# Kernel optimization log

Hardware: AMD Instinct MI355X
Metric: run time of the kernel (lower is better)

## Reference

```python
import jax, jax.numpy as jnp
import numpy as np

B, S, D, H, HD = 1, 2048, 3072, 24, 128
FFN = int(D / 3 * 8)  # 8192
ADALN = 256
NORM_EPS = 1e-6
QK_EPS = 1e-5
AXES_DIMS = (16, 56, 56)
AXES_LENS = (64, 128, 128)
THETA = 256.0


def rmsnorm(x, w, eps):
    var = jnp.mean(jnp.square(x), axis=-1, keepdims=True)
    return x * jax.lax.rsqrt(var + eps) * w


def apply_rope(x, cos, sin):
    # x: [B,S,H,HD]; cos/sin: [B,S,HD//2] (broadcast over heads, matching freqs_cis.unsqueeze(2))
    xr = x[..., 0::2]
    xi = x[..., 1::2]
    c = cos[:, :, None, :]
    s = sin[:, :, None, :]
    or_ = xr * c - xi * s
    oi_ = xr * s + xi * c
    return jnp.stack([or_, oi_], axis=-1).reshape(x.shape)


def rope_angles(ids):
    # ids: [B,S,3] int; returns angles [B,S,HD//2] concatenated per axis like RopeEmbedder
    parts = []
    for d, idx_axis in zip(AXES_DIMS, range(len(AXES_DIMS))):
        freqs = 1.0 / (THETA ** (jnp.arange(0, d, 2, dtype=jnp.float32) / d))  # [d/2]
        ang = ids[..., idx_axis].astype(jnp.float32)[..., None] * freqs  # [B,S,d/2]
        parts.append(ang)
    return jnp.concatenate(parts, axis=-1)  # [B,S,64]


def setup_inputs() -> dict:
    key = jax.random.key(0)
    ks = jax.random.split(key, 20)
    w = 0.02
    ids = jnp.concatenate([
        jax.random.randint(ks[15], (B, S, 1), 0, AXES_LENS[0]),
        jax.random.randint(ks[16], (B, S, 1), 0, AXES_LENS[1]),
        jax.random.randint(ks[17], (B, S, 1), 0, AXES_LENS[2]),
    ], axis=-1)
    return {
        "x": jax.random.normal(ks[0], (B, S, D), jnp.float32),
        "adaln_input": jax.random.normal(ks[1], (B, ADALN), jnp.float32),
        "attn_mask": jnp.ones((B, S), dtype=bool),
        "ids": ids,
        "attn_norm1_w": jnp.ones((D,), jnp.float32),
        "attn_norm2_w": jnp.ones((D,), jnp.float32),
        "ffn_norm1_w": jnp.ones((D,), jnp.float32),
        "ffn_norm2_w": jnp.ones((D,), jnp.float32),
        "norm_q_w": jnp.ones((HD,), jnp.float32),
        "norm_k_w": jnp.ones((HD,), jnp.float32),
        "wq": jax.random.normal(ks[2], (D, D), jnp.float32) * w,
        "wk": jax.random.normal(ks[3], (D, D), jnp.float32) * w,
        "wv": jax.random.normal(ks[4], (D, D), jnp.float32) * w,
        "wo": jax.random.normal(ks[5], (D, D), jnp.float32) * w,
        "w1": jax.random.normal(ks[6], (D, FFN), jnp.float32) * w,
        "w2": jax.random.normal(ks[7], (FFN, D), jnp.float32) * w,
        "w3": jax.random.normal(ks[8], (D, FFN), jnp.float32) * w,
        "adaln_w": jax.random.normal(ks[9], (ADALN, 4 * D), jnp.float32) * w,
        "adaln_b": jnp.zeros((4 * D,), jnp.float32),
    }


def block_forward(x, adaln_input, attn_mask, ids,
                  attn_norm1_w, attn_norm2_w, ffn_norm1_w, ffn_norm2_w,
                  norm_q_w, norm_k_w, wq, wk, wv, wo, w1, w2, w3,
                  adaln_w, adaln_b):
    ang = rope_angles(ids)
    cos, sin = jnp.cos(ang), jnp.sin(ang)

    mod = adaln_input @ adaln_w + adaln_b
    scale_msa, gate_msa, scale_mlp, gate_mlp = jnp.split(mod[:, None, :], 4, axis=2)
    gate_msa, gate_mlp = jnp.tanh(gate_msa), jnp.tanh(gate_mlp)
    scale_msa, scale_mlp = 1.0 + scale_msa, 1.0 + scale_mlp

    # Attention branch
    xs = rmsnorm(x, attn_norm1_w, NORM_EPS) * scale_msa  # [B,S,D]
    q = (xs @ wq).reshape(B, S, H, HD)
    k = (xs @ wk).reshape(B, S, H, HD)
    v = (xs @ wv).reshape(B, S, H, HD)
    q = rmsnorm(q, norm_q_w, QK_EPS)
    k = rmsnorm(k, norm_k_w, QK_EPS)
    q = apply_rope(q, cos, sin)
    k = apply_rope(k, cos, sin)

    scores = jnp.einsum('bqhd,bkhd->bhqk', q, k) / jnp.sqrt(jnp.float32(HD))
    neg = jnp.finfo(scores.dtype).min
    scores = jnp.where(attn_mask[:, None, None, :], scores, neg)
    probs = jax.nn.softmax(scores, axis=-1)
    attn = jnp.einsum('bhqk,bkhd->bqhd', probs, v).reshape(B, S, D)
    attn_out = attn @ wo

    x = x + gate_msa * rmsnorm(attn_out, attn_norm2_w, NORM_EPS)

    # FFN branch (SwiGLU)
    xf = rmsnorm(x, ffn_norm1_w, NORM_EPS) * scale_mlp
    h = jax.nn.silu(xf @ w1) * (xf @ w3)
    ffn_out = h @ w2
    x = x + gate_mlp * rmsnorm(ffn_out, ffn_norm2_w, NORM_EPS)
    return x


def reference(x, adaln_input, attn_mask, ids,
              attn_norm1_w, attn_norm2_w, ffn_norm1_w, ffn_norm2_w,
              norm_q_w, norm_k_w, wq, wk, wv, wo, w1, w2, w3,
              adaln_w, adaln_b):
    return block_forward(x, adaln_input, attn_mask, ids,
                         attn_norm1_w, attn_norm2_w, ffn_norm1_w, ffn_norm2_w,
                         norm_q_w, norm_k_w, wq, wk, wv, wo, w1, w2, w3,
                         adaln_w, adaln_b)
```

## Files before the change

### kernel.cpp

```cpp
#include <hip/hip_runtime.h>

#define AS1 __attribute__((address_space(1)))
#define AS3 __attribute__((address_space(3)))

typedef __bf16 bf16;
using bf16x8 = __attribute__((ext_vector_type(8))) __bf16;
using bf16x4 = __attribute__((ext_vector_type(4))) __bf16;
using bf16x2 = __attribute__((ext_vector_type(2))) __bf16;
using f32x4  = __attribute__((ext_vector_type(4))) float;


__device__ inline float wsum(float v) {
#pragma unroll
  for (int o = 32; o; o >>= 1) v += __shfl_xor(v, o, 64);
  return v;
}

template <int EPI>
__global__ __launch_bounds__(512, 1) void gemm256(
    const bf16* __restrict__ A, const bf16* __restrict__ Bt, void* __restrict__ Cv,
    int K, int lda, int ldb, int ldc, long long kOff, long long sC) {
  __shared__ bf16 lds[2][2][256 * 64];
  const int t = threadIdx.x;
  const int lane = t & 63, wid = t >> 6;
  const int wm = wid >> 2, wn = wid & 3;
  const int row16 = lane & 15, kg = lane >> 4;
  const int m0 = blockIdx.x * 256, n0 = blockIdx.y * 256;
  const int NT = K >> 6;
  const int sgran = (lane & 7) ^ (lane >> 3);
  A += (long long)blockIdx.z * kOff;
  Bt += (long long)blockIdx.z * kOff;

  auto stageA = [&](int buf, int r, int tk) {
    const int wrow = ((wid & 4) << 5) + (r << 5) + ((wid & 3) << 3);
    __builtin_amdgcn_global_load_lds(
        (const AS1 void*)(A + (long long)(m0 + wrow + (lane >> 3)) * lda + tk * 64 +
                          (sgran << 3)),
        (AS3 void*)&lds[buf][0][wrow * 64], 16, 0, 0);
  };
  auto stageB = [&](int buf, int r, int tk) {
    const int wrow = ((wid & 4) << 5) + (r << 5) + ((wid & 3) << 3);
    __builtin_amdgcn_global_load_lds(
        (const AS1 void*)(Bt + (long long)(n0 + wrow + (lane >> 3)) * ldb + tk * 64 +
                          (sgran << 3)),
        (AS3 void*)&lds[buf][1][wrow * 64], 16, 0, 0);
  };

  f32x4 acc[8][4];
#pragma unroll
  for (int i = 0; i < 8; ++i)
#pragma unroll
    for (int j = 0; j < 4; ++j) acc[i][j] = (f32x4){0.f, 0.f, 0.f, 0.f};

#pragma unroll
  for (int r = 0; r < 4; ++r) { stageA(0, r, 0); stageB(0, r, 0); }
#pragma unroll
  for (int r = 0; r < 3; ++r) { stageA(1, r, 1); stageB(1, r, 1); }

  bf16x8 bfr[4][2], af[2][2];

  for (int kt = 0; kt < NT; ++kt) {
    const int cb = kt & 1, nb = cb ^ 1;
    if (kt + 1 < NT) asm volatile("s_waitcnt vmcnt(6)" ::: "memory");
    else             asm volatile("s_waitcnt vmcnt(0)" ::: "memory");
    __builtin_amdgcn_s_barrier();

    if (kt + 1 < NT) { stageA(nb, 3, kt + 1); stageB(nb, 3, kt + 1); }
#pragma unroll
    for (int ni = 0; ni < 4; ++ni)
#pragma unroll
      for (int kk = 0; kk < 2; ++kk) {
        const int r = wn * 64 + ni * 16 + row16;
        bfr[ni][kk] = *(const bf16x8*)&lds[cb][1][r * 64 + (((kk * 4 + kg) ^ (r & 7)) << 3)];
      }
#pragma unroll
    for (int mi = 0; mi < 2; ++mi)
#pragma unroll
      for (int kk = 0; kk < 2; ++kk) {
        const int r = wm * 128 + mi * 16 + row16;
        af[mi][kk] = *(const bf16x8*)&lds[cb][0][r * 64 + (((kk * 4 + kg) ^ (r & 7)) << 3)];
      }
    asm volatile("s_waitcnt lgkmcnt(0)" ::: "memory");
    __builtin_amdgcn_s_setprio(1);
#pragma unroll
    for (int kk = 0; kk < 2; ++kk)
#pragma unroll
      for (int mi = 0; mi < 2; ++mi)
#pragma unroll
        for (int ni = 0; ni < 4; ++ni)
          acc[mi][ni] =
              __builtin_amdgcn_mfma_f32_16x16x32_bf16(af[mi][kk], bfr[ni][kk], acc[mi][ni], 0, 0, 0);
    __builtin_amdgcn_s_setprio(0);

#pragma unroll
    for (int q = 1; q < 4; ++q) {
      __builtin_amdgcn_s_barrier();
      if (kt + 2 < NT) { stageA(cb, q - 1, kt + 2); stageB(cb, q - 1, kt + 2); }
#pragma unroll
      for (int mi = 0; mi < 2; ++mi)
#pragma unroll
        for (int kk = 0; kk < 2; ++kk) {
          const int r = wm * 128 + q * 32 + mi * 16 + row16;
          af[mi][kk] = *(const bf16x8*)&lds[cb][0][r * 64 + (((kk * 4 + kg) ^ (r & 7)) << 3)];
        }
      asm volatile("s_waitcnt lgkmcnt(0)" ::: "memory");
      __builtin_amdgcn_s_setprio(1);
#pragma unroll
      for (int kk = 0; kk < 2; ++kk)
#pragma unroll
        for (int mi = 0; mi < 2; ++mi)
#pragma unroll
          for (int ni = 0; ni < 4; ++ni)
            acc[q * 2 + mi][ni] = __builtin_amdgcn_mfma_f32_16x16x32_bf16(
                af[mi][kk], bfr[ni][kk], acc[q * 2 + mi][ni], 0, 0, 0);
      __builtin_amdgcn_s_setprio(0);
    }
  }

  float* Cf = (float*)Cv;
  bf16* Cb = (bf16*)Cv;
  const long long cz = (long long)blockIdx.z * sC;
#pragma unroll
  for (int mf = 0; mf < 8; ++mf)
#pragma unroll
    for (int ni = 0; ni < 4; ++ni)
#pragma unroll
      for (int rr = 0; rr < 4; ++rr) {
        const int row = m0 + wm * 128 + (mf >> 1) * 32 + (mf & 1) * 16 + kg * 4 + rr;
        const int col = n0 + wn * 64 + ni * 16 + row16;
        const float v = acc[mf][ni][rr];
        if constexpr (EPI == 2) {
          const float other = __shfl_xor(v, 1, 64);
          if ((row16 & 1) == 0) {
            const float sl = v / (1.f + __expf(-v));
            Cb[cz + (long long)row * ldc + (col >> 1)] = (bf16)(sl * other);
          }
        } else {
          const long long idx = cz + (long long)row * ldc + col;
          if constexpr (EPI == 0) Cf[idx] = v;
          else Cb[idx] = (bf16)v;
        }
      }
}

template <int EPI>
__global__ __launch_bounds__(512, 1) void gemm192(
    const bf16* __restrict__ A, const bf16* __restrict__ Bt, void* __restrict__ Cv,
    int K, int lda, int ldb, int ldc, long long kOff, long long sC) {
  __shared__ bf16 lds[2][448 * 64];
  const int t = threadIdx.x;
  const int lane = t & 63, wid = t >> 6;
  const int wm = wid >> 2, wn = wid & 3;
  const int row16 = lane & 15, kg = lane >> 4;
  const int m0 = blockIdx.x * 256, n0 = blockIdx.y * 192;
  const int NT = K >> 6;
  const int sgran = (lane & 7) ^ (lane >> 3);
  A += (long long)blockIdx.z * kOff;
  Bt += (long long)blockIdx.z * kOff;

  auto stageA = [&](int buf, int r, int tk) {
    const int wrow = ((wid & 4) << 5) + (r << 5) + ((wid & 3) << 3);
    __builtin_amdgcn_global_load_lds(
        (const AS1 void*)(A + (long long)(m0 + wrow + (lane >> 3)) * lda + tk * 64 +
                          (sgran << 3)),
        (AS3 void*)&lds[buf][wrow * 64], 16, 0, 0);
  };
  auto stageB = [&](int buf, int r, int tk) {
    const int wrow = r * 64 + wid * 8;
    __builtin_amdgcn_global_load_lds(
        (const AS1 void*)(Bt + (long long)(n0 + wrow + (lane >> 3)) * ldb + tk * 64 +
                          (sgran << 3)),
        (AS3 void*)&lds[buf][(256 + wrow) * 64], 16, 0, 0);
  };

  f32x4 acc[8][3];
#pragma unroll
  for (int i = 0; i < 8; ++i)
#pragma unroll
    for (int j = 0; j < 3; ++j) acc[i][j] = (f32x4){0.f, 0.f, 0.f, 0.f};

#pragma unroll
  for (int r = 0; r < 4; ++r) stageA(0, r, 0);
#pragma unroll
  for (int r = 0; r < 3; ++r) stageB(0, r, 0);
#pragma unroll
  for (int r = 0; r < 3; ++r) { stageA(1, r, 1); stageB(1, r, 1); }

  bf16x8 bfr[3][2], af[2][2];

  for (int kt = 0; kt < NT; ++kt) {
    const int cb = kt & 1, nb = cb ^ 1;
    if (kt + 1 < NT) asm volatile("s_waitcnt vmcnt(6)" ::: "memory");
    else             asm volatile("s_waitcnt vmcnt(0)" ::: "memory");
    __builtin_amdgcn_s_barrier();

    if (kt + 1 < NT) stageA(nb, 3, kt + 1);
#pragma unroll
    for (int ni = 0; ni < 3; ++ni)
#pragma unroll
      for (int kk = 0; kk < 2; ++kk) {
        const int r = wn * 48 + ni * 16 + row16;
        bfr[ni][kk] =
            *(const bf16x8*)&lds[cb][(256 + r) * 64 + (((kk * 4 + kg) ^ (r & 7)) << 3)];
      }
#pragma unroll
    for (int mi = 0; mi < 2; ++mi)
#pragma unroll
      for (int kk = 0; kk < 2; ++kk) {
        const int r = wm * 128 + mi * 16 + row16;
        af[mi][kk] = *(const bf16x8*)&lds[cb][r * 64 + (((kk * 4 + kg) ^ (r & 7)) << 3)];
      }
    __builtin_amdgcn_s_barrier();
    asm volatile("s_waitcnt lgkmcnt(0)" ::: "memory");
    __builtin_amdgcn_s_setprio(1);
#pragma unroll
    for (int kk = 0; kk < 2; ++kk)
#pragma unroll
      for (int mi = 0; mi < 2; ++mi)
#pragma unroll
        for (int ni = 0; ni < 3; ++ni)
          acc[mi][ni] =
              __builtin_amdgcn_mfma_f32_16x16x32_bf16(af[mi][kk], bfr[ni][kk], acc[mi][ni], 0, 0, 0);
    __builtin_amdgcn_s_setprio(0);

#pragma unroll
    for (int q = 1; q < 4; ++q) {
      __builtin_amdgcn_s_barrier();
      if (kt + 2 < NT) { stageA(cb, q - 1, kt + 2); stageB(cb, q - 1, kt + 2); }
#pragma unroll
      for (int mi = 0; mi < 2; ++mi)
#pragma unroll
        for (int kk = 0; kk < 2; ++kk) {
          const int r = wm * 128 + q * 32 + mi * 16 + row16;
          af[mi][kk] = *(const bf16x8*)&lds[cb][r * 64 + (((kk * 4 + kg) ^ (r & 7)) << 3)];
        }
      __builtin_amdgcn_s_barrier();
      asm volatile("s_waitcnt lgkmcnt(0)" ::: "memory");
      __builtin_amdgcn_s_setprio(1);
#pragma unroll
      for (int kk = 0; kk < 2; ++kk)
#pragma unroll
        for (int mi = 0; mi < 2; ++mi)
#pragma unroll
          for (int ni = 0; ni < 3; ++ni)
            acc[q * 2 + mi][ni] = __builtin_amdgcn_mfma_f32_16x16x32_bf16(
                af[mi][kk], bfr[ni][kk], acc[q * 2 + mi][ni], 0, 0, 0);
      __builtin_amdgcn_s_setprio(0);
    }
  }

  float* Cf = (float*)Cv;
  bf16* Cb = (bf16*)Cv;
  const long long cz = (long long)blockIdx.z * sC;
#pragma unroll
  for (int mf = 0; mf < 8; ++mf)
#pragma unroll
    for (int ni = 0; ni < 3; ++ni)
#pragma unroll
      for (int rr = 0; rr < 4; ++rr) {
        const int row = m0 + wm * 128 + (mf >> 1) * 32 + (mf & 1) * 16 + kg * 4 + rr;
        const int col = n0 + wn * 48 + ni * 16 + row16;
        const long long idx = cz + (long long)row * ldc + col;
        const float v = acc[mf][ni][rr];
        if constexpr (EPI == 0) Cf[idx] = v;
        else Cb[idx] = (bf16)v;
      }
}

__global__ __launch_bounds__(256) void flash_attn_k(const bf16* __restrict__ qkv,
                                                    const bf16* __restrict__ vt,
                                                    bf16* __restrict__ Opb,
                                                    float* __restrict__ mlp) {
  __shared__ bf16 Ks[64 * 128];
  __shared__ bf16 Vs[128 * 64];
  __shared__ bf16 Ps[4 * 32 * 64];
  const int t = threadIdx.x, lane = t & 63, wid = t >> 6;
  const int row16 = lane & 15, kg = lane >> 4;
  const int q0 = blockIdx.x * 128;
  const int h = blockIdx.y;
  const int z = blockIdx.z;
  const bf16* Qp = qkv + h * 128;
  const bf16* Kp = qkv + 3072 + h * 128;
  const bf16* Vt = vt + (long long)h * 262144;
  const float iscale = 0.08838834764831845f;

  bf16x8 qf[2][4];
#pragma unroll
  for (int mi = 0; mi < 2; ++mi)
#pragma unroll
    for (int kc = 0; kc < 4; ++kc)
      qf[mi][kc] = *(const bf16x8*)&Qp[(long long)(q0 + wid * 32 + mi * 16 + row16) * 9216 +
                                       kc * 32 + kg * 8];
  bf16x8 ones;
#pragma unroll
  for (int j = 0; j < 8; ++j) ones[j] = (bf16)1.0f;

  f32x4 oacc[2][8];
#pragma unroll
  for (int mi = 0; mi < 2; ++mi)
#pragma unroll
    for (int nd = 0; nd < 8; ++nd) oacc[mi][nd] = (f32x4){0.f, 0.f, 0.f, 0.f};
  f32x4 lacc[2] = {(f32x4){0.f, 0.f, 0.f, 0.f}, (f32x4){0.f, 0.f, 0.f, 0.f}};
  float mst[2][4];
#pragma unroll
  for (int mi = 0; mi < 2; ++mi)
#pragma unroll
    for (int r = 0; r < 4; ++r) mst[mi][r] = -1e30f;

  bf16* Pw = &Ps[wid * 2048];
  const int kvbase = z << 10;

  for (int kv0 = kvbase; kv0 < kvbase + 1024; kv0 += 64) {
#pragma unroll
    for (int p = 0; p < 4; ++p) {
      const int gi = p * 256 + t;
      const int row = gi >> 4, g = gi & 15;
      __builtin_amdgcn_global_load_lds(
          (const AS1 void*)(Kp + (long long)(kv0 + row) * 9216 + ((g ^ (row & 7)) << 3)),
          (AS3 void*)&Ks[(p * 256 + wid * 64) * 8], 16, 0, 0);
    }
#pragma unroll
    for (int p = 0; p < 4; ++p) {
      const int gi = p * 256 + t;
      const int row = gi >> 3, g = gi & 7;
      __builtin_amdgcn_global_load_lds(
          (const AS1 void*)(Vt + (long long)row * 2048 + kv0 + ((g ^ (row & 7)) << 3)),
          (AS3 void*)&Vs[(p * 256 + wid * 64) * 8], 16, 0, 0);
    }
    __syncthreads();

    f32x4 sacc[2][4];
#pragma unroll
    for (int mi = 0; mi < 2; ++mi)
#pragma unroll
      for (int nf = 0; nf < 4; ++nf) sacc[mi][nf] = (f32x4){0.f, 0.f, 0.f, 0.f};
#pragma unroll
    for (int kc = 0; kc < 4; ++kc) {
      bf16x8 kf[4];
#pragma unroll
      for (int nf = 0; nf < 4; ++nf) {
        const int row = nf * 16 + row16;
        kf[nf] = *(const bf16x8*)&Ks[(row * 16 + ((kc * 4 + kg) ^ (row & 7))) * 8];
      }
#pragma unroll
      for (int mi = 0; mi < 2; ++mi)
#pragma unroll
        for (int nf = 0; nf < 4; ++nf)
          sacc[mi][nf] =
              __builtin_amdgcn_mfma_f32_16x16x32_bf16(qf[mi][kc], kf[nf], sacc[mi][nf], 0, 0, 0);
    }

    float fac[2][4];
#pragma unroll
    for (int mi = 0; mi < 2; ++mi)
#pragma unroll
      for (int r = 0; r < 4; ++r) {
        float rm = sacc[mi][0][r];
#pragma unroll
        for (int nf = 1; nf < 4; ++nf) rm = fmaxf(rm, sacc[mi][nf][r]);
        rm = fmaxf(rm, __shfl_xor(rm, 1, 64));
        rm = fmaxf(rm, __shfl_xor(rm, 2, 64));
        rm = fmaxf(rm, __shfl_xor(rm, 4, 64));
        rm = fmaxf(rm, __shfl_xor(rm, 8, 64));
        const float mnew = fmaxf(mst[mi][r], rm * iscale);
        fac[mi][r] = __expf(mst[mi][r] - mnew);
        mst[mi][r] = mnew;
#pragma unroll
        for (int nf = 0; nf < 4; ++nf)
          sacc[mi][nf][r] = __expf(sacc[mi][nf][r] * iscale - mnew);
      }
#pragma unroll
    for (int mi = 0; mi < 2; ++mi)
#pragma unroll
      for (int r = 0; r < 4; ++r) {
        lacc[mi][r] *= fac[mi][r];
#pragma unroll
        for (int nd = 0; nd < 8; ++nd) oacc[mi][nd][r] *= fac[mi][r];
      }

#pragma unroll
    for (int mi = 0; mi < 2; ++mi)
#pragma unroll
      for (int nf = 0; nf < 4; ++nf)
#pragma unroll
        for (int r = 0; r < 4; ++r) {
          const int row = mi * 16 + kg * 4 + r;
          const int col = nf * 16 + row16;
          Pw[(row * 8 + ((col >> 3) ^ (row & 7))) * 8 + (col & 7)] = (bf16)sacc[mi][nf][r];
        }

#pragma unroll
    for (int kvc = 0; kvc < 2; ++kvc) {
      bf16x8 pf[2], vf[8];
#pragma unroll
      for (int mi = 0; mi < 2; ++mi) {
        const int row = mi * 16 + row16;
        pf[mi] = *(const bf16x8*)&Pw[(row * 8 + ((kvc * 4 + kg) ^ (row & 7))) * 8];
      }
#pragma unroll
      for (int nd = 0; nd < 8; ++nd) {
        const int row = nd * 16 + row16;
        vf[nd] = *(const bf16x8*)&Vs[(row * 8 + ((kvc * 4 + kg) ^ (row & 7))) * 8];
      }
#pragma unroll
      for (int mi = 0; mi < 2; ++mi) {
        lacc[mi] = __builtin_amdgcn_mfma_f32_16x16x32_bf16(pf[mi], ones, lacc[mi], 0, 0, 0);
#pragma unroll
        for (int nd = 0; nd < 8; ++nd)
          oacc[mi][nd] =
              __builtin_amdgcn_mfma_f32_16x16x32_bf16(pf[mi], vf[nd], oacc[mi][nd], 0, 0, 0);
      }
    }
    __syncthreads();
  }

  bf16* Oz = Opb + (long long)z * 6291456;
#pragma unroll
  for (int mi = 0; mi < 2; ++mi)
#pragma unroll
    for (int nd = 0; nd < 8; ++nd)
#pragma unroll
      for (int r = 0; r < 4; ++r) {
        const int row = q0 + wid * 32 + mi * 16 + kg * 4 + r;
        const int col = h * 128 + nd * 16 + row16;
        Oz[(long long)row * 3072 + col] = (bf16)oacc[mi][nd][r];
      }
  if (row16 == 0) {
#pragma unroll
    for (int mi = 0; mi < 2; ++mi)
#pragma unroll
      for (int r = 0; r < 4; ++r) {
        const int s = q0 + wid * 32 + mi * 16 + kg * 4 + r;
        const long long mi2 = ((long long)z * 49152 + s * 24 + h) * 2;
        mlp[mi2] = mst[mi][r];
        mlp[mi2 + 1] = lacc[mi][r];
      }
  }
}

__global__ __launch_bounds__(256) void fa_combine_k(const bf16* __restrict__ Opb,
                                                    const float* __restrict__ mlp,
                                                    bf16* __restrict__ attn) {
  const int t = threadIdx.x, lane = t & 63, wid = t >> 6;
  const int pair = blockIdx.x * 4 + wid;
  const int s = pair / 24, h = pair % 24;
  const float2 ml0 = *(const float2*)&mlp[(long long)pair * 2];
  const float2 ml1 = *(const float2*)&mlp[(49152LL + pair) * 2];
  const float m = fmaxf(ml0.x, ml1.x);
  const float a0 = __expf(ml0.x - m), a1 = __expf(ml1.x - m);
  const float inv = 1.f / (ml0.y * a0 + ml1.y * a1);
  const long long base = (long long)s * 3072 + h * 128 + lane * 2;
  const bf16x2 o0 = *(const bf16x2*)&Opb[base];
  const bf16x2 o1 = *(const bf16x2*)&Opb[6291456LL + base];
  bf16x2 o;
  o[0] = (bf16)(((float)o0[0] * a0 + (float)o1[0] * a1) * inv);
  o[1] = (bf16)(((float)o0[1] * a0 + (float)o1[1] * a1) * inv);
  *(bf16x2*)&attn[base] = o;
}

__device__ inline void convT_tile(const float* __restrict__ in, bf16* __restrict__ out,
                                  int R, int C, int bx, int by, int rmul, int roff) {
  __shared__ float tile[64][65];
  const int t = threadIdx.x;
  const int r0 = by * 64, c0 = bx * 64;
#pragma unroll
  for (int it = 0; it < 4; ++it) {
    const int idx = it * 256 + t;
    const int rl = idx >> 4, c4 = (idx & 15) << 2;
    const float4 v = *(const float4*)&in[(long long)(r0 + rl) * C + c0 + c4];
    tile[rl][c4 + 0] = v.x;
    tile[rl][c4 + 1] = v.y;
    tile[rl][c4 + 2] = v.z;
    tile[rl][c4 + 3] = v.w;
  }
  __syncthreads();
#pragma unroll
  for (int it = 0; it < 4; ++it) {
    const int idx = it * 256 + t;
    const int cl = idx >> 4, r4 = (idx & 15) << 2;
    bf16x4 o;
    o[0] = (bf16)tile[r4 + 0][cl];
    o[1] = (bf16)tile[r4 + 1][cl];
    o[2] = (bf16)tile[r4 + 2][cl];
    o[3] = (bf16)tile[r4 + 3][cl];
    *(bf16x4*)&out[(long long)((c0 + cl) * rmul + roff) * R + r0 + r4] = o;
  }
}

__global__ __launch_bounds__(256) void convAll(
    const float* __restrict__ wq, const float* __restrict__ wk,
    const float* __restrict__ wv, const float* __restrict__ wo,
    const float* __restrict__ w1, const float* __restrict__ w3,
    const float* __restrict__ w2, bf16* __restrict__ wqkvT, bf16* __restrict__ woT,
    bf16* __restrict__ w13T, bf16* __restrict__ w2T) {
  const int id = blockIdx.x;
  if (id < 9216) {
    const int m = id / 2304, l = id % 2304;
    const float* in = m == 0 ? wq : m == 1 ? wk : m == 2 ? wv : wo;
    bf16* out = m < 3 ? wqkvT + (long long)m * 9437184 : woT;
    convT_tile(in, out, 3072, 3072, l % 48, l / 48, 1, 0);
  } else if (id < 21504) {
    int l = id - 9216;
    const int m = l / 6144;
    l %= 6144;
    convT_tile(m ? w3 : w1, w13T, 3072, 8192, l % 128, l / 128, 2, m);
  } else {
    const int l = id - 21504;
    convT_tile(w2, w2T, 8192, 3072, l % 48, l / 48, 1, 0);
  }
}

__global__ __launch_bounds__(256) void ropetab_k(const int* __restrict__ ids,
                                                 float* __restrict__ cosT,
                                                 float* __restrict__ sinT) {
  const int i = blockIdx.x * 256 + threadIdx.x;
  const int s = i >> 6, j = i & 63;
  int ax, fi;
  float d;
  if (j < 8) { ax = 0; fi = j; d = 16.f; }
  else if (j < 36) { ax = 1; fi = j - 8; d = 56.f; }
  else { ax = 2; fi = j - 36; d = 56.f; }
  const float freq = exp2f(-16.f * (float)fi / d);
  const float ang = (float)ids[s * 3 + ax] * freq;
  cosT[i] = cosf(ang);
  sinT[i] = sinf(ang);
}

__global__ __launch_bounds__(256) void adaln_kernel(const float* __restrict__ ain,
                                                    const float* __restrict__ W,
                                                    const float* __restrict__ b,
                                                    float* __restrict__ out) {
  __shared__ float a[256];
  const int t = threadIdx.x;
  a[t] = ain[t];
  __syncthreads();
  const int n = blockIdx.x * 256 + t;
  float acc = b[n];
  for (int k = 0; k < 256; ++k) acc = fmaf(a[k], W[(long long)k * 12288 + n], acc);
  const int chunk = n / 3072;
  out[n] = (chunk & 1) ? tanhf(acc) : (1.f + acc);
}

__global__ __launch_bounds__(256) void rmsnorm_scale_k(const float* __restrict__ x,
                                                       const float* __restrict__ w,
                                                       const float* __restrict__ scale,
                                                       bf16* __restrict__ out) {
  __shared__ float red[4];
  const int t = threadIdx.x, lane = t & 63, wid = t >> 6;
  const long long base = (long long)blockIdx.x * 3072;
  float v[12];
  float ss = 0.f;
#pragma unroll
  for (int ch = 0; ch < 3; ++ch) {
    const float4 f = *(const float4*)&x[base + ch * 1024 + t * 4];
    v[ch * 4 + 0] = f.x; v[ch * 4 + 1] = f.y; v[ch * 4 + 2] = f.z; v[ch * 4 + 3] = f.w;
    ss += f.x * f.x + f.y * f.y + f.z * f.z + f.w * f.w;
  }
  ss = wsum(ss);
  if (!lane) red[wid] = ss;
  __syncthreads();
  const float r = rsqrtf((red[0] + red[1] + red[2] + red[3]) / 3072.f + 1e-6f);
#pragma unroll
  for (int ch = 0; ch < 3; ++ch) {
    const int col = ch * 1024 + t * 4;
    bf16x4 o;
#pragma unroll
    for (int j = 0; j < 4; ++j) o[j] = (bf16)(v[ch * 4 + j] * r * w[col + j] * scale[col + j]);
    *(bf16x4*)&out[base + col] = o;
  }
}

__global__ __launch_bounds__(256) void qknorm_rope_k(bf16* __restrict__ qkv,
                                                     const float* __restrict__ cosT,
                                                     const float* __restrict__ sinT,
                                                     const float* __restrict__ wq,
                                                     const float* __restrict__ wk) {
  const int t = threadIdx.x, lane = t & 63, wid = t >> 6;
  const int idx = blockIdx.x * 4 + wid;
  const int s = idx / 24, h = idx % 24;
  const int isK = blockIdx.y;
  bf16* base = qkv + (long long)s * 9216 + isK * 3072 + h * 128;
  bf16x2 p = *(const bf16x2*)(base + 2 * lane);
  float xr = (float)p[0], xi = (float)p[1];
  const float ss = wsum(xr * xr + xi * xi);
  const float r = rsqrtf(ss / 128.f + 1e-5f);
  const float* w = isK ? wk : wq;
  const float2 wv = *(const float2*)&w[2 * lane];
  xr *= r * wv.x;
  xi *= r * wv.y;
  const float c = cosT[s * 64 + lane], sn = sinT[s * 64 + lane];
  bf16x2 o;
  o[0] = (bf16)(xr * c - xi * sn);
  o[1] = (bf16)(xr * sn + xi * c);
  *(bf16x2*)(base + 2 * lane) = o;
}

__global__ __launch_bounds__(256) void vtrans_k(const bf16* __restrict__ qkv,
                                                bf16* __restrict__ vt) {
  __shared__ bf16 tile[64][72];
  const int t = threadIdx.x;
  const int s0 = blockIdx.x * 64, d0 = blockIdx.y * 64, h = blockIdx.z;
#pragma unroll
  for (int it = 0; it < 2; ++it) {
    const int idx = it * 256 + t;
    const int sl = idx >> 3, c8 = (idx & 7) << 3;
    const bf16x8 v =
        *(const bf16x8*)&qkv[(long long)(s0 + sl) * 9216 + 6144 + h * 128 + d0 + c8];
    *(bf16x8*)&tile[sl][c8] = v;
  }
  __syncthreads();
#pragma unroll
  for (int it = 0; it < 2; ++it) {
    const int idx = it * 256 + t;
    const int dl = idx >> 3, s8 = (idx & 7) << 3;
    bf16x8 o;
#pragma unroll
    for (int j = 0; j < 8; ++j) o[j] = tile[s8 + j][dl];
    *(bf16x8*)&vt[(long long)h * 262144 + (long long)(d0 + dl) * 2048 + s0 + s8] = o;
  }
}

__global__ __launch_bounds__(256) void resid1_k(
    const float* __restrict__ x, const float* __restrict__ p0, const float* __restrict__ p1,
    const float* __restrict__ n2w, const float* __restrict__ gate,
    const float* __restrict__ f1w, const float* __restrict__ smlp,
    float* __restrict__ x1, bf16* __restrict__ xf) {
  __shared__ float red[8];
  const int t = threadIdx.x, lane = t & 63, wid = t >> 6;
  const long long base = (long long)blockIdx.x * 3072;
  float av[12];
  float ss = 0.f;
#pragma unroll
  for (int ch = 0; ch < 3; ++ch) {
    const float4 f0 = *(const float4*)&p0[base + ch * 1024 + t * 4];
    const float4 f1 = *(const float4*)&p1[base + ch * 1024 + t * 4];
    const float a0 = f0.x + f1.x, a1 = f0.y + f1.y, a2 = f0.z + f1.z, a3 = f0.w + f1.w;
    av[ch * 4 + 0] = a0; av[ch * 4 + 1] = a1; av[ch * 4 + 2] = a2; av[ch * 4 + 3] = a3;
    ss += a0 * a0 + a1 * a1 + a2 * a2 + a3 * a3;
  }
  ss = wsum(ss);
  if (!lane) red[wid] = ss;
  __syncthreads();
  const float r = rsqrtf((red[0] + red[1] + red[2] + red[3]) / 3072.f + 1e-6f);
  float xv[12];
  float ss2 = 0.f;
#pragma unroll
  for (int ch = 0; ch < 3; ++ch) {
    const int col = ch * 1024 + t * 4;
    const float4 f = *(const float4*)&x[base + col];
    float4 o;
    o.x = f.x + gate[col + 0] * (av[ch * 4 + 0] * r * n2w[col + 0]);
    o.y = f.y + gate[col + 1] * (av[ch * 4 + 1] * r * n2w[col + 1]);
    o.z = f.z + gate[col + 2] * (av[ch * 4 + 2] * r * n2w[col + 2]);
    o.w = f.w + gate[col + 3] * (av[ch * 4 + 3] * r * n2w[col + 3]);
    *(float4*)&x1[base + col] = o;
    xv[ch * 4 + 0] = o.x; xv[ch * 4 + 1] = o.y; xv[ch * 4 + 2] = o.z; xv[ch * 4 + 3] = o.w;
    ss2 += o.x * o.x + o.y * o.y + o.z * o.z + o.w * o.w;
  }
  ss2 = wsum(ss2);
  if (!lane) red[4 + wid] = ss2;
  __syncthreads();
  const float r2 = rsqrtf((red[4] + red[5] + red[6] + red[7]) / 3072.f + 1e-6f);
#pragma unroll
  for (int ch = 0; ch < 3; ++ch) {
    const int col = ch * 1024 + t * 4;
    bf16x4 o;
#pragma unroll
    for (int j = 0; j < 4; ++j)
      o[j] = (bf16)(xv[ch * 4 + j] * r2 * f1w[col + j] * smlp[col + j]);
    *(bf16x4*)&xf[base + col] = o;
  }
}

__global__ __launch_bounds__(256) void resid2_k(const float* __restrict__ x1,
                                                const float* __restrict__ f0,
                                                const float* __restrict__ f1,
                                                const float* __restrict__ nw,
                                                const float* __restrict__ gate,
                                                float* __restrict__ out) {
  __shared__ float red[4];
  const int t = threadIdx.x, lane = t & 63, wid = t >> 6;
  const long long base = (long long)blockIdx.x * 3072;
  float fv[12];
  float ss = 0.f;
#pragma unroll
  for (int ch = 0; ch < 3; ++ch) {
    const float4 a = *(const float4*)&f0[base + ch * 1024 + t * 4];
    const float4 b = *(const float4*)&f1[base + ch * 1024 + t * 4];
    const float a0 = a.x + b.x, a1 = a.y + b.y, a2 = a.z + b.z, a3 = a.w + b.w;
    fv[ch * 4 + 0] = a0; fv[ch * 4 + 1] = a1; fv[ch * 4 + 2] = a2; fv[ch * 4 + 3] = a3;
    ss += a0 * a0 + a1 * a1 + a2 * a2 + a3 * a3;
  }
  ss = wsum(ss);
  if (!lane) red[wid] = ss;
  __syncthreads();
  const float r = rsqrtf((red[0] + red[1] + red[2] + red[3]) / 3072.f + 1e-6f);
#pragma unroll
  for (int ch = 0; ch < 3; ++ch) {
    const int col = ch * 1024 + t * 4;
    const float4 f = *(const float4*)&x1[base + col];
    float4 o;
    o.x = f.x + gate[col + 0] * (fv[ch * 4 + 0] * r * nw[col + 0]);
    o.y = f.y + gate[col + 1] * (fv[ch * 4 + 1] * r * nw[col + 1]);
    o.z = f.z + gate[col + 2] * (fv[ch * 4 + 2] * r * nw[col + 2]);
    o.w = f.w + gate[col + 3] * (fv[ch * 4 + 3] * r * nw[col + 3]);
    *(float4*)&out[base + col] = o;
  }
}

extern "C" void kernel_launch(void* const* d_in, const int* in_sizes, int n_in,
                              void* d_out, int out_size, void* d_ws, size_t ws_size,
                              hipStream_t stream) {
  const float* x    = (const float*)d_in[0];
  const float* ain  = (const float*)d_in[1];
  const int* ids    = (const int*)d_in[3];
  const float* n1w  = (const float*)d_in[4];
  const float* n2w  = (const float*)d_in[5];
  const float* fn1w = (const float*)d_in[6];
  const float* fn2w = (const float*)d_in[7];
  const float* nqw  = (const float*)d_in[8];
  const float* nkw  = (const float*)d_in[9];
  const float* wq   = (const float*)d_in[10];
  const float* wk   = (const float*)d_in[11];
  const float* wv   = (const float*)d_in[12];
  const float* wo   = (const float*)d_in[13];
  const float* w1   = (const float*)d_in[14];
  const float* w2   = (const float*)d_in[15];
  const float* w3   = (const float*)d_in[16];
  const float* adw  = (const float*)d_in[17];
  const float* adb  = (const float*)d_in[18];

  if (ws_size < 395362304ULL) return;

  char* ws = (char*)d_ws;
  bf16* wqkvT = (bf16*)(ws + 0LL);
  bf16* woT   = (bf16*)(ws + 56623104LL);
  bf16* w13T  = (bf16*)(ws + 75497472LL);
  bf16* w2T   = (bf16*)(ws + 176160768LL);
  float* cosT = (float*)(ws + 226492416LL);
  float* sinT = (float*)(ws + 227016704LL);
  float* adv  = (float*)(ws + 227540992LL);
  bf16* xs    = (bf16*)(ws + 227590144LL);
  char* big   = ws + 240173056LL;
  float* x1   = (float*)(big);
  bf16* qkv   = (bf16*)(big + 25165824LL);
  bf16* vt    = (bf16*)(big + 62914560LL);
  bf16* attn  = (bf16*)(big + 75497472LL);
  bf16* Opb   = (bf16*)(big + 88080384LL);
  float* aoP  = (float*)(big + 88080384LL);
  float* mlp  = (float*)(big + 138412032LL);
  bf16* hbuf  = (bf16*)(big + 92274688LL);
  float* ffnP = (float*)(big + 25165824LL);

  const dim3 b256(256);
  const dim3 b512(512);

  ropetab_k<<<dim3(512), b256, 0, stream>>>(ids, cosT, sinT);
  adaln_kernel<<<dim3(48), b256, 0, stream>>>(ain, adw, adb, adv);

  convAll<<<dim3(27648), b256, 0, stream>>>(wq, wk, wv, wo, w1, w3, w2, wqkvT, woT, w13T,
                                            w2T);

  rmsnorm_scale_k<<<dim3(2048), b256, 0, stream>>>(x, n1w, adv, xs);

  gemm192<1><<<dim3(8, 48, 1), b512, 0, stream>>>(xs, wqkvT, qkv, 3072, 3072, 3072, 9216,
                                                  0LL, 0LL);

  qknorm_rope_k<<<dim3(12288, 2), b256, 0, stream>>>(qkv, cosT, sinT, nqw, nkw);
  vtrans_k<<<dim3(32, 2, 24), b256, 0, stream>>>(qkv, vt);

  flash_attn_k<<<dim3(16, 24, 2), b256, 0, stream>>>(qkv, vt, Opb, mlp);
  fa_combine_k<<<dim3(12288), b256, 0, stream>>>(Opb, mlp, attn);

  gemm192<0><<<dim3(8, 16, 2), b512, 0, stream>>>(attn, woT, aoP, 1536, 3072, 3072, 3072,
                                                  1536LL, 6291456LL);
  resid1_k<<<dim3(2048), b256, 0, stream>>>(x, aoP, aoP + 6291456LL, n2w, adv + 3072, fn1w,
                                            adv + 6144, x1, xs);
  gemm256<2><<<dim3(8, 64, 1), b512, 0, stream>>>(xs, w13T, hbuf, 3072, 3072, 3072, 8192,
                                                  0LL, 0LL);
  gemm192<0><<<dim3(8, 16, 2), b512, 0, stream>>>(hbuf, w2T, ffnP, 4096, 8192, 8192, 3072,
                                                  4096LL, 6291456LL);
  resid2_k<<<dim3(2048), b256, 0, stream>>>(x1, ffnP, ffnP + 6291456LL, fn2w, adv + 9216,
                                            (float*)d_out);
}
```

Before: 832.0 us.

## Add 128x192 QKV GEMM kernel and interleave w1/w3 in 16-column blocks

Replaces the QKV projection GEMM (256x192 tiles, 384 blocks) with a new gemmQ kernel using 128x192 tiles and 768 blocks, which gives better CU occupancy and wave balance on the 256-CU device. The w1/w3 weight transpose now interleaves in 16-row groups rather than alternating single rows. The SwiGLU epilogue can then pair silu and gate values from adjacent accumulator fragments instead of using a cross-lane shuffle with half the lanes idle. The smaller tiles trade some operand reuse for more parallelism.

```diff
diff --git a/kernel.cpp b/kernel.cpp
--- a/kernel.cpp
+++ b/kernel.cpp
@@ -120,27 +120,35 @@
   float* Cf = (float*)Cv;
   bf16* Cb = (bf16*)Cv;
   const long long cz = (long long)blockIdx.z * sC;
-#pragma unroll
-  for (int mf = 0; mf < 8; ++mf)
-#pragma unroll
-    for (int ni = 0; ni < 4; ++ni)
-#pragma unroll
-      for (int rr = 0; rr < 4; ++rr) {
-        const int row = m0 + wm * 128 + (mf >> 1) * 32 + (mf & 1) * 16 + kg * 4 + rr;
-        const int col = n0 + wn * 64 + ni * 16 + row16;
-        const float v = acc[mf][ni][rr];
-        if constexpr (EPI == 2) {
-          const float other = __shfl_xor(v, 1, 64);
-          if ((row16 & 1) == 0) {
-            const float sl = v / (1.f + __expf(-v));
-            Cb[cz + (long long)row * ldc + (col >> 1)] = (bf16)(sl * other);
-          }
-        } else {
+  if constexpr (EPI == 2) {
+#pragma unroll
+    for (int mf = 0; mf < 8; ++mf)
+#pragma unroll
+      for (int np = 0; np < 2; ++np)
+#pragma unroll
+        for (int rr = 0; rr < 4; ++rr) {
+          const int row = m0 + wm * 128 + (mf >> 1) * 32 + (mf & 1) * 16 + kg * 4 + rr;
+          const int col = (n0 >> 1) + wn * 32 + np * 16 + row16;
+          const float a = acc[mf][np * 2][rr];
+          const float b = acc[mf][np * 2 + 1][rr];
+          const float sl = a / (1.f + __expf(-a));
+          Cb[cz + (long long)row * ldc + col] = (bf16)(sl * b);
+        }
+  } else {
+#pragma unroll
+    for (int mf = 0; mf < 8; ++mf)
+#pragma unroll
+      for (int ni = 0; ni < 4; ++ni)
+#pragma unroll
+        for (int rr = 0; rr < 4; ++rr) {
+          const int row = m0 + wm * 128 + (mf >> 1) * 32 + (mf & 1) * 16 + kg * 4 + rr;
+          const int col = n0 + wn * 64 + ni * 16 + row16;
           const long long idx = cz + (long long)row * ldc + col;
+          const float v = acc[mf][ni][rr];
           if constexpr (EPI == 0) Cf[idx] = v;
           else Cb[idx] = (bf16)v;
         }
-      }
+  }
 }
 
 template <int EPI>
@@ -264,6 +272,96 @@
         const float v = acc[mf][ni][rr];
         if constexpr (EPI == 0) Cf[idx] = v;
         else Cb[idx] = (bf16)v;
+      }
+}
+
+__global__ __launch_bounds__(512, 1) void gemmQ(
+    const bf16* __restrict__ A, const bf16* __restrict__ Bt, bf16* __restrict__ C,
+    int K, int lda, int ldb, int ldc) {
+  __shared__ bf16 lds[2][320 * 64];
+  const int t = threadIdx.x;
+  const int lane = t & 63, wid = t >> 6;
+  const int wm = wid >> 1, wn = wid & 1;
+  const int row16 = lane & 15, kg = lane >> 4;
+  const int m0 = blockIdx.x * 128, n0 = blockIdx.y * 192;
+  const int NT = K >> 6;
+  const int sgran = (lane & 7) ^ (lane >> 3);
+
+  auto stageA = [&](int buf, int r, int tk) {
+    const int wrow = r * 64 + wid * 8;
+    __builtin_amdgcn_global_load_lds(
+        (const AS1 void*)(A + (long long)(m0 + wrow + (lane >> 3)) * lda + tk * 64 +
+                          (sgran << 3)),
+        (AS3 void*)&lds[buf][wrow * 64], 16, 0, 0);
+  };
+  auto stageB = [&](int buf, int r, int tk) {
+    const int wrow = r * 64 + wid * 8;
+    __builtin_amdgcn_global_load_lds(
+        (const AS1 void*)(Bt + (long long)(n0 + wrow + (lane >> 3)) * ldb + tk * 64 +
+                          (sgran << 3)),
+        (AS3 void*)&lds[buf][(128 + wrow) * 64], 16, 0, 0);
+  };
+
+  f32x4 acc[2][6];
+#pragma unroll
+  for (int i = 0; i < 2; ++i)
+#pragma unroll
+    for (int j = 0; j < 6; ++j) acc[i][j] = (f32x4){0.f, 0.f, 0.f, 0.f};
+
+#pragma unroll
+  for (int r = 0; r < 2; ++r) stageA(0, r, 0);
+#pragma unroll
+  for (int r = 0; r < 3; ++r) stageB(0, r, 0);
+
+  bf16x8 af[2][2], bfr[6][2];
+
+  for (int kt = 0; kt < NT; ++kt) {
+    const int cb = kt & 1, nb = cb ^ 1;
+    asm volatile("s_waitcnt vmcnt(0)" ::: "memory");
+    __builtin_amdgcn_s_barrier();
+    if (kt + 1 < NT) {
+#pragma unroll
+      for (int r = 0; r < 2; ++r) stageA(nb, r, kt + 1);
+#pragma unroll
+      for (int r = 0; r < 3; ++r) stageB(nb, r, kt + 1);
+    }
+#pragma unroll
+    for (int mi = 0; mi < 2; ++mi)
+#pragma unroll
+      for (int kk = 0; kk < 2; ++kk) {
+        const int r = wm * 32 + mi * 16 + row16;
+        af[mi][kk] = *(const bf16x8*)&lds[cb][r * 64 + (((kk * 4 + kg) ^ (r & 7)) << 3)];
+      }
+#pragma unroll
+    for (int ni = 0; ni < 6; ++ni)
+#pragma unroll
+      for (int kk = 0; kk < 2; ++kk) {
+        const int r = wn * 96 + ni * 16 + row16;
+        bfr[ni][kk] =
+            *(const bf16x8*)&lds[cb][(128 + r) * 64 + (((kk * 4 + kg) ^ (r & 7)) << 3)];
+      }
+    asm volatile("s_waitcnt lgkmcnt(0)" ::: "memory");
+    __builtin_amdgcn_s_setprio(1);
+#pragma unroll
+    for (int kk = 0; kk < 2; ++kk)
+#pragma unroll
+      for (int mi = 0; mi < 2; ++mi)
+#pragma unroll
+        for (int ni = 0; ni < 6; ++ni)
+          acc[mi][ni] =
+              __builtin_amdgcn_mfma_f32_16x16x32_bf16(af[mi][kk], bfr[ni][kk], acc[mi][ni], 0, 0, 0);
+    __builtin_amdgcn_s_setprio(0);
+  }
+
+#pragma unroll
+  for (int mi = 0; mi < 2; ++mi)
+#pragma unroll
+    for (int ni = 0; ni < 6; ++ni)
+#pragma unroll
+      for (int rr = 0; rr < 4; ++rr) {
+        const int row = m0 + wm * 32 + mi * 16 + kg * 4 + rr;
+        const int col = n0 + wn * 96 + ni * 16 + row16;
+        C[(long long)row * ldc + col] = (bf16)acc[mi][ni][rr];
       }
 }
 
@@ -459,7 +557,8 @@
 }
 
 __device__ inline void convT_tile(const float* __restrict__ in, bf16* __restrict__ out,
-                                  int R, int C, int bx, int by, int rmul, int roff) {
+                                  int R, int C, int bx, int by, int interleave16,
+                                  int roff) {
   __shared__ float tile[64][65];
   const int t = threadIdx.x;
   const int r0 = by * 64, c0 = bx * 64;
@@ -483,7 +582,10 @@
     o[1] = (bf16)tile[r4 + 1][cl];
     o[2] = (bf16)tile[r4 + 2][cl];
     o[3] = (bf16)tile[r4 + 3][cl];
-    *(bf16x4*)&out[(long long)((c0 + cl) * rmul + roff) * R + r0 + r4] = o;
+    const long long orow = interleave16 ? (long long)(c0 * 2 + ((cl >> 4) << 5) +
+                                                      (cl & 15) + roff)
+                                        : (long long)(c0 + cl);
+    *(bf16x4*)&out[orow * R + r0 + r4] = o;
   }
 }
 
@@ -498,15 +600,15 @@
     const int m = id / 2304, l = id % 2304;
     const float* in = m == 0 ? wq : m == 1 ? wk : m == 2 ? wv : wo;
     bf16* out = m < 3 ? wqkvT + (long long)m * 9437184 : woT;
-    convT_tile(in, out, 3072, 3072, l % 48, l / 48, 1, 0);
+    convT_tile(in, out, 3072, 3072, l % 48, l / 48, 0, 0);
   } else if (id < 21504) {
     int l = id - 9216;
     const int m = l / 6144;
     l %= 6144;
-    convT_tile(m ? w3 : w1, w13T, 3072, 8192, l % 128, l / 128, 2, m);
+    convT_tile(m ? w3 : w1, w13T, 3072, 8192, l % 128, l / 128, 1, m * 16);
   } else {
     const int l = id - 21504;
-    convT_tile(w2, w2T, 8192, 3072, l % 48, l / 48, 1, 0);
+    convT_tile(w2, w2T, 8192, 3072, l % 48, l / 48, 0, 0);
   }
 }
 
@@ -763,8 +865,7 @@
 
   rmsnorm_scale_k<<<dim3(2048), b256, 0, stream>>>(x, n1w, adv, xs);
 
-  gemm192<1><<<dim3(8, 48, 1), b512, 0, stream>>>(xs, wqkvT, qkv, 3072, 3072, 3072, 9216,
-                                                  0LL, 0LL);
+  gemmQ<<<dim3(16, 48), b512, 0, stream>>>(xs, wqkvT, qkv, 3072, 3072, 3072, 9216);
 
   qknorm_rope_k<<<dim3(12288, 2), b256, 0, stream>>>(qkv, cosT, sinT, nqw, nkw);
   vtrans_k<<<dim3(32, 2, 24), b256, 0, stream>>>(qkv, vt);
```

Result: no change. 831.8 us (-0.0%).

## Store split-K GEMM partials in bf16 and block-interleave w1/w3 for SwiGLU epilogue

Applied to the files above, without the earlier changes.

The split-K partial outputs of the wo and w2 GEMMs are now written as bf16 instead of fp32, and the residual kernels read bf16 partials. This halves the partial-buffer write and read traffic. The w1/w3 transposed weights are interleaved in blocks of 16 rows instead of alternating rows, so each thread holds matching gate and up values in its own accumulators. That removes the cross-lane shuffle and the idle half-lanes in the SwiGLU epilogue. The cost is extra rounding from storing partial sums in bf16, and the hbuf offset is moved to avoid overlapping the resized buffers.

```diff
diff --git a/kernel.cpp b/kernel.cpp
--- a/kernel.cpp
+++ b/kernel.cpp
@@ -120,27 +120,35 @@
   float* Cf = (float*)Cv;
   bf16* Cb = (bf16*)Cv;
   const long long cz = (long long)blockIdx.z * sC;
-#pragma unroll
-  for (int mf = 0; mf < 8; ++mf)
-#pragma unroll
-    for (int ni = 0; ni < 4; ++ni)
-#pragma unroll
-      for (int rr = 0; rr < 4; ++rr) {
-        const int row = m0 + wm * 128 + (mf >> 1) * 32 + (mf & 1) * 16 + kg * 4 + rr;
-        const int col = n0 + wn * 64 + ni * 16 + row16;
-        const float v = acc[mf][ni][rr];
-        if constexpr (EPI == 2) {
-          const float other = __shfl_xor(v, 1, 64);
-          if ((row16 & 1) == 0) {
-            const float sl = v / (1.f + __expf(-v));
-            Cb[cz + (long long)row * ldc + (col >> 1)] = (bf16)(sl * other);
-          }
-        } else {
+  if constexpr (EPI == 2) {
+#pragma unroll
+    for (int mf = 0; mf < 8; ++mf)
+#pragma unroll
+      for (int np = 0; np < 2; ++np)
+#pragma unroll
+        for (int rr = 0; rr < 4; ++rr) {
+          const int row = m0 + wm * 128 + (mf >> 1) * 32 + (mf & 1) * 16 + kg * 4 + rr;
+          const int col = (n0 >> 1) + wn * 32 + np * 16 + row16;
+          const float a = acc[mf][np * 2][rr];
+          const float b = acc[mf][np * 2 + 1][rr];
+          const float sl = a / (1.f + __expf(-a));
+          Cb[cz + (long long)row * ldc + col] = (bf16)(sl * b);
+        }
+  } else {
+#pragma unroll
+    for (int mf = 0; mf < 8; ++mf)
+#pragma unroll
+      for (int ni = 0; ni < 4; ++ni)
+#pragma unroll
+        for (int rr = 0; rr < 4; ++rr) {
+          const int row = m0 + wm * 128 + (mf >> 1) * 32 + (mf & 1) * 16 + kg * 4 + rr;
+          const int col = n0 + wn * 64 + ni * 16 + row16;
           const long long idx = cz + (long long)row * ldc + col;
+          const float v = acc[mf][ni][rr];
           if constexpr (EPI == 0) Cf[idx] = v;
           else Cb[idx] = (bf16)v;
         }
-      }
+  }
 }
 
 template <int EPI>
@@ -459,7 +467,8 @@
 }
 
 __device__ inline void convT_tile(const float* __restrict__ in, bf16* __restrict__ out,
-                                  int R, int C, int bx, int by, int rmul, int roff) {
+                                  int R, int C, int bx, int by, int interleave16,
+                                  int roff) {
   __shared__ float tile[64][65];
   const int t = threadIdx.x;
   const int r0 = by * 64, c0 = bx * 64;
@@ -483,7 +492,10 @@
     o[1] = (bf16)tile[r4 + 1][cl];
     o[2] = (bf16)tile[r4 + 2][cl];
     o[3] = (bf16)tile[r4 + 3][cl];
-    *(bf16x4*)&out[(long long)((c0 + cl) * rmul + roff) * R + r0 + r4] = o;
+    const long long orow = interleave16 ? (long long)(c0 * 2 + ((cl >> 4) << 5) +
+                                                      (cl & 15) + roff)
+                                        : (long long)(c0 + cl);
+    *(bf16x4*)&out[orow * R + r0 + r4] = o;
   }
 }
 
@@ -498,15 +510,15 @@
     const int m = id / 2304, l = id % 2304;
     const float* in = m == 0 ? wq : m == 1 ? wk : m == 2 ? wv : wo;
     bf16* out = m < 3 ? wqkvT + (long long)m * 9437184 : woT;
-    convT_tile(in, out, 3072, 3072, l % 48, l / 48, 1, 0);
+    convT_tile(in, out, 3072, 3072, l % 48, l / 48, 0, 0);
   } else if (id < 21504) {
     int l = id - 9216;
     const int m = l / 6144;
     l %= 6144;
-    convT_tile(m ? w3 : w1, w13T, 3072, 8192, l % 128, l / 128, 2, m);
+    convT_tile(m ? w3 : w1, w13T, 3072, 8192, l % 128, l / 128, 1, m * 16);
   } else {
     const int l = id - 21504;
-    convT_tile(w2, w2T, 8192, 3072, l % 48, l / 48, 1, 0);
+    convT_tile(w2, w2T, 8192, 3072, l % 48, l / 48, 0, 0);
   }
 }
 
@@ -621,7 +633,7 @@
 }
 
 __global__ __launch_bounds__(256) void resid1_k(
-    const float* __restrict__ x, const float* __restrict__ p0, const float* __restrict__ p1,
+    const float* __restrict__ x, const bf16* __restrict__ p0, const bf16* __restrict__ p1,
     const float* __restrict__ n2w, const float* __restrict__ gate,
     const float* __restrict__ f1w, const float* __restrict__ smlp,
     float* __restrict__ x1, bf16* __restrict__ xf) {
@@ -632,11 +644,14 @@
   float ss = 0.f;
 #pragma unroll
   for (int ch = 0; ch < 3; ++ch) {
-    const float4 f0 = *(const float4*)&p0[base + ch * 1024 + t * 4];
-    const float4 f1 = *(const float4*)&p1[base + ch * 1024 + t * 4];
-    const float a0 = f0.x + f1.x, a1 = f0.y + f1.y, a2 = f0.z + f1.z, a3 = f0.w + f1.w;
-    av[ch * 4 + 0] = a0; av[ch * 4 + 1] = a1; av[ch * 4 + 2] = a2; av[ch * 4 + 3] = a3;
-    ss += a0 * a0 + a1 * a1 + a2 * a2 + a3 * a3;
+    const bf16x4 f0 = *(const bf16x4*)&p0[base + ch * 1024 + t * 4];
+    const bf16x4 f1 = *(const bf16x4*)&p1[base + ch * 1024 + t * 4];
+#pragma unroll
+    for (int j = 0; j < 4; ++j) {
+      const float a = (float)f0[j] + (float)f1[j];
+      av[ch * 4 + j] = a;
+      ss += a * a;
+    }
   }
   ss = wsum(ss);
   if (!lane) red[wid] = ss;
@@ -673,8 +688,8 @@
 }
 
 __global__ __launch_bounds__(256) void resid2_k(const float* __restrict__ x1,
-                                                const float* __restrict__ f0,
-                                                const float* __restrict__ f1,
+                                                const bf16* __restrict__ f0,
+                                                const bf16* __restrict__ f1,
                                                 const float* __restrict__ nw,
                                                 const float* __restrict__ gate,
                                                 float* __restrict__ out) {
@@ -685,11 +700,14 @@
   float ss = 0.f;
 #pragma unroll
   for (int ch = 0; ch < 3; ++ch) {
-    const float4 a = *(const float4*)&f0[base + ch * 1024 + t * 4];
-    const float4 b = *(const float4*)&f1[base + ch * 1024 + t * 4];
-    const float a0 = a.x + b.x, a1 = a.y + b.y, a2 = a.z + b.z, a3 = a.w + b.w;
-    fv[ch * 4 + 0] = a0; fv[ch * 4 + 1] = a1; fv[ch * 4 + 2] = a2; fv[ch * 4 + 3] = a3;
-    ss += a0 * a0 + a1 * a1 + a2 * a2 + a3 * a3;
+    const bf16x4 a = *(const bf16x4*)&f0[base + ch * 1024 + t * 4];
+    const bf16x4 b = *(const bf16x4*)&f1[base + ch * 1024 + t * 4];
+#pragma unroll
+    for (int j = 0; j < 4; ++j) {
+      const float v = (float)a[j] + (float)b[j];
+      fv[ch * 4 + j] = v;
+      ss += v * v;
+    }
   }
   ss = wsum(ss);
   if (!lane) red[wid] = ss;
@@ -747,10 +765,10 @@
   bf16* vt    = (bf16*)(big + 62914560LL);
   bf16* attn  = (bf16*)(big + 75497472LL);
   bf16* Opb   = (bf16*)(big + 88080384LL);
-  float* aoP  = (float*)(big + 88080384LL);
+  bf16* aoP   = (bf16*)(big + 88080384LL);
   float* mlp  = (float*)(big + 138412032LL);
-  bf16* hbuf  = (bf16*)(big + 92274688LL);
-  float* ffnP = (float*)(big + 25165824LL);
+  bf16* hbuf  = (bf16*)(big + 121634816LL);
+  bf16* ffnP  = (bf16*)(big + 25165824LL);
 
   const dim3 b256(256);
   const dim3 b512(512);
@@ -772,13 +790,13 @@
   flash_attn_k<<<dim3(16, 24, 2), b256, 0, stream>>>(qkv, vt, Opb, mlp);
   fa_combine_k<<<dim3(12288), b256, 0, stream>>>(Opb, mlp, attn);
 
-  gemm192<0><<<dim3(8, 16, 2), b512, 0, stream>>>(attn, woT, aoP, 1536, 3072, 3072, 3072,
+  gemm192<1><<<dim3(8, 16, 2), b512, 0, stream>>>(attn, woT, aoP, 1536, 3072, 3072, 3072,
                                                   1536LL, 6291456LL);
   resid1_k<<<dim3(2048), b256, 0, stream>>>(x, aoP, aoP + 6291456LL, n2w, adv + 3072, fn1w,
                                             adv + 6144, x1, xs);
   gemm256<2><<<dim3(8, 64, 1), b512, 0, stream>>>(xs, w13T, hbuf, 3072, 3072, 3072, 8192,
                                                   0LL, 0LL);
-  gemm192<0><<<dim3(8, 16, 2), b512, 0, stream>>>(hbuf, w2T, ffnP, 4096, 8192, 8192, 3072,
+  gemm192<1><<<dim3(8, 16, 2), b512, 0, stream>>>(hbuf, w2T, ffnP, 4096, 8192, 8192, 3072,
                                                   4096LL, 6291456LL);
   resid2_k<<<dim3(2048), b256, 0, stream>>>(x1, ffnP, ffnP + 6291456LL, fn2w, adv + 9216,
                                             (float*)d_out);
```

Measured after the change: 805.6 us (median of 2 runs). 1.03x faster.
